# Kernel optimization log

Hardware: AMD Instinct MI355X
Metric: run time of the kernel (lower is better)

The kernel has to match this reference:

```python
import jax, jax.numpy as jnp
import numpy as np

N_NODES = 100000
N_EDGES = 1600000
IN_F, HID_F, OUT_F = 128, 128, 64


def setup_inputs() -> dict:
    key = jax.random.key(0)
    ks = jax.random.split(key, 8)
    x = jax.random.normal(ks[0], (N_NODES, IN_F), dtype=jnp.float32)
    edge_index = jax.random.randint(ks[1], (2, N_EDGES), 0, N_NODES, dtype=jnp.int64)
    w1 = jax.random.normal(ks[2], (IN_F, HID_F), dtype=jnp.float32) * 0.05
    b1 = jax.random.normal(ks[3], (HID_F,), dtype=jnp.float32) * 0.05
    c1 = jax.random.normal(ks[4], (IN_F, HID_F, 3), dtype=jnp.float32) * 0.01
    w2 = jax.random.normal(ks[5], (HID_F, OUT_F), dtype=jnp.float32) * 0.05
    b2 = jax.random.normal(ks[6], (OUT_F,), dtype=jnp.float32) * 0.05
    c2 = jax.random.normal(ks[7], (IN_F, OUT_F, 3), dtype=jnp.float32) * 0.01
    return {"x": x, "edge_index": edge_index, "w1": w1, "b1": b1, "c1": c1,
            "w2": w2, "b2": b2, "c2": c2}


def _minimal_kan(x, w, b, c):
    # linear term: (N, out)
    lin = x @ w + b
    # polynomial basis (x, x^2, x^3): (N, in, 3)
    basis = jnp.stack([x, x * x, x * x * x], axis=-1)
    # fused contraction over (in, 3); same math as the (N,in,out,3) broadcast-sum
    kan_out = jnp.einsum('nib,iob->no', basis, c)
    return lin + 0.1 * kan_out


def _aggregate(h, source, target, num_nodes):
    # mean over incoming messages, degree clamped at 1
    deg = jax.ops.segment_sum(jnp.ones(source.shape[0], dtype=h.dtype), target,
                              num_segments=num_nodes)
    deg = jnp.maximum(deg, 1.0)
    out = jax.ops.segment_sum(h[source], target, num_segments=num_nodes)
    return out / deg[:, None]


def reference(x, edge_index, w1, b1, c1, w2, b2, c2):
    source, target = edge_index[0], edge_index[1]
    n = x.shape[0]
    h = _minimal_kan(x, w1, b1, c1)
    h = jax.nn.relu(h)
    h = _aggregate(h, source, target, n)
    h = _minimal_kan(h, w2, b2, c2)
    h = _aggregate(h, source, target, n)
    return jax.nn.log_softmax(h, axis=-1)
```

## Files before the change

### kernel.cpp

```cpp
#include <hip/hip_runtime.h>
#include <hip/hip_bf16.h>
#include <math.h>

#define N_NODES 100000
#define N_EDGES 1600000
#define IN_F 128
#define HID_F 128
#define OUT_F 64
#define BSTX 136

#define BK_BITS 8
#define BK_SIZE 256
#define NBUCK ((N_NODES + BK_SIZE - 1) / BK_SIZE)
#define EPB 4096
#define NBLK_SORT ((N_EDGES + EPB - 1) / EPB)
#define BCAP 5120
#define PCAP (BCAP + 7 * BK_SIZE)
#define PK_SRC_MASK 0xffffffu
#define PAD8(d) (((d) + 7) & ~7)

#define K1T ((N_NODES + 63) / 64)
#define K1A 781
#define K1B (K1T - K1A)

#define K1_LDS (64 * BSTX * 2)
#define A_LDS 19520

typedef __attribute__((ext_vector_type(8))) short s8v;
typedef __attribute__((ext_vector_type(4))) short s4v;
typedef __attribute__((ext_vector_type(4))) float f4v;
typedef __attribute__((ext_vector_type(2))) float f2v;

__device__ __forceinline__ short f2bf(float f) {
    __hip_bfloat16 h = __float2bfloat16(f);
    return __builtin_bit_cast(short, h);
}
__device__ __forceinline__ float bf2f(short s) {
    return __builtin_bit_cast(float, ((unsigned)(unsigned short)s) << 16);
}

__global__ __launch_bounds__(256) void fold_weights_bf16(
    const float* __restrict__ w1, const float* __restrict__ c1,
    const float* __restrict__ w2, const float* __restrict__ c2,
    short* __restrict__ Wb1, short* __restrict__ Wb2,
    unsigned* __restrict__ h1d, unsigned* __restrict__ h2d,
    int* __restrict__ bcur)
{
    if (blockIdx.x == 0) {
        if (threadIdx.x < 32) h1d[(size_t)N_NODES * 32 + threadIdx.x] = 0;
        if (threadIdx.x < 16) h2d[(size_t)N_NODES * 16 + threadIdx.x] = 0;
        for (int i = threadIdx.x; i < NBUCK; i += 256) bcur[i] = i * BCAP;
    }
    int idx = blockIdx.x * 256 + threadIdx.x;
    if (idx < 384 * HID_F) {
        int k = idx >> 7, n = idx & 127;
        int p = k >> 7, f = k & 127;
        int si = f * HID_F + n;
        float v = (p == 0) ? (w1[si] + 0.1f * c1[si * 3])
                           : 0.1f * c1[si * 3 + p];
        Wb1[(((k >> 3) * HID_F) + n) * 8 + (k & 7)] = f2bf(v);
    } else {
        idx -= 384 * HID_F;
        if (idx < 384 * OUT_F) {
            int k = idx >> 6, n = idx & 63;
            int p = k >> 7, f = k & 127;
            int si = f * OUT_F + n;
            float v = (p == 0) ? (w2[si] + 0.1f * c2[si * 3])
                               : 0.1f * c2[si * 3 + p];
            Wb2[(((k >> 3) * OUT_F) + n) * 8 + (k & 7)] = f2bf(v);
        }
    }
}

__device__ __forceinline__ void kan1_body(
    short* sb, int node0,
    const float* __restrict__ x, const short* __restrict__ Wb,
    const float* __restrict__ bias, unsigned* __restrict__ h1d)
{
    const int tid  = threadIdx.x;
    const int lane = tid & 63;
    const int wave = tid >> 6;
    const int q = lane >> 4, r = lane & 15;

#pragma unroll
    for (int it = 0; it < 8; ++it) {
        int idx = tid + 256 * it;
        int m = idx >> 5, c4 = (idx & 31) * 4;
        int gm = min(node0 + m, N_NODES - 1);
        float4 v = *(const float4*)(x + (size_t)gm * IN_F + c4);
        s4v p0;
        p0[0] = f2bf(v.x); p0[1] = f2bf(v.y);
        p0[2] = f2bf(v.z); p0[3] = f2bf(v.w);
        *(s4v*)(sb + m * BSTX + c4) = p0;
    }
    __syncthreads();

    const int wm = (wave & 1) * 32;
    const int wn = (wave >> 1) * 64;

    f4v acc[2][4];
#pragma unroll
    for (int i = 0; i < 2; ++i)
#pragma unroll
        for (int j = 0; j < 4; ++j)
            acc[i][j] = (f4v){0.f, 0.f, 0.f, 0.f};

    float bj[4];
#pragma unroll
    for (int j = 0; j < 4; ++j) bj[j] = bias[wn + j * 16 + r];

#pragma unroll
    for (int kc = 0; kc < 4; ++kc) {
        const int col = kc * 32 + q * 8;
        s8v a0[2];
        float xf[2][8], x2[2][8];
#pragma unroll
        for (int i = 0; i < 2; ++i) {
            a0[i] = *(const s8v*)(sb + (wm + i * 16 + r) * BSTX + col);
#pragma unroll
            for (int t = 0; t < 8; ++t) xf[i][t] = bf2f(a0[i][t]);
        }
#pragma unroll
        for (int j = 0; j < 4; ++j) {
            const s8v b = *(const s8v*)(Wb + (((kc * 4 + q) * HID_F) + wn + j * 16 + r) * 8);
            acc[0][j] = __builtin_amdgcn_mfma_f32_16x16x32_bf16(a0[0], b, acc[0][j], 0, 0, 0);
            acc[1][j] = __builtin_amdgcn_mfma_f32_16x16x32_bf16(a0[1], b, acc[1][j], 0, 0, 0);
        }
        s8v a1[2];
#pragma unroll
        for (int i = 0; i < 2; ++i)
#pragma unroll
            for (int t = 0; t < 8; ++t) {
                x2[i][t] = xf[i][t] * xf[i][t];
                a1[i][t] = f2bf(x2[i][t]);
            }
#pragma unroll
        for (int j = 0; j < 4; ++j) {
            const s8v b = *(const s8v*)(Wb + ((((4 + kc) * 4 + q) * HID_F) + wn + j * 16 + r) * 8);
            acc[0][j] = __builtin_amdgcn_mfma_f32_16x16x32_bf16(a1[0], b, acc[0][j], 0, 0, 0);
            acc[1][j] = __builtin_amdgcn_mfma_f32_16x16x32_bf16(a1[1], b, acc[1][j], 0, 0, 0);
        }
        s8v a2[2];
#pragma unroll
        for (int i = 0; i < 2; ++i)
#pragma unroll
            for (int t = 0; t < 8; ++t)
                a2[i][t] = f2bf(x2[i][t] * xf[i][t]);
#pragma unroll
        for (int j = 0; j < 4; ++j) {
            const s8v b = *(const s8v*)(Wb + ((((8 + kc) * 4 + q) * HID_F) + wn + j * 16 + r) * 8);
            acc[0][j] = __builtin_amdgcn_mfma_f32_16x16x32_bf16(a2[0], b, acc[0][j], 0, 0, 0);
            acc[1][j] = __builtin_amdgcn_mfma_f32_16x16x32_bf16(a2[1], b, acc[1][j], 0, 0, 0);
        }
    }

    const int dci = ((wn >> 6) << 4) + r;
#pragma unroll
    for (int i = 0; i < 2; ++i)
#pragma unroll
        for (int e = 0; e < 4; ++e) {
            int grow = node0 + wm + i * 16 + q * 4 + e;
            if (grow < N_NODES) {
                float v0 = fmaxf(acc[i][0][e] + bj[0], 0.f);
                float v1 = fmaxf(acc[i][1][e] + bj[1], 0.f);
                float v2 = fmaxf(acc[i][2][e] + bj[2], 0.f);
                float v3 = fmaxf(acc[i][3][e] + bj[3], 0.f);
                int pk = __builtin_amdgcn_cvt_pk_fp8_f32(v0, v1, 0, false);
                pk = __builtin_amdgcn_cvt_pk_fp8_f32(v2, v3, pk, true);
                h1d[(size_t)grow * 32 + dci] = (unsigned)pk;
            }
        }
}

__global__ __launch_bounds__(256) void scatter_kan1(
    const int* __restrict__ src, const int* __restrict__ tgt,
    int* __restrict__ bcur, unsigned* __restrict__ spk,
    const float* __restrict__ x, const short* __restrict__ Wb,
    const float* __restrict__ bias, unsigned* __restrict__ h1d)
{
    __shared__ __align__(16) char smem[A_LDS];
    const int tid = threadIdx.x;

    if (blockIdx.x < NBLK_SORT) {
        int* h    = (int*)smem;
        int* base = h + NBUCK;
        int* tg   = base + NBUCK;
        for (int i = tid; i < NBUCK; i += 256) h[i] = 0;
        __syncthreads();
        int e0 = blockIdx.x * EPB;
        int n = min(EPB, N_EDGES - e0);
        for (int i = tid; i < n; i += 256) {
            int t = tgt[e0 + i];
            tg[i] = t;
            atomicAdd(&h[t >> BK_BITS], 1);
        }
        __syncthreads();
        for (int i = tid; i < NBUCK; i += 256) {
            int c = h[i];
            base[i] = c ? atomicAdd(&bcur[i], c) : 0;
            h[i] = 0;
        }
        __syncthreads();
        for (int i = tid; i < n; i += 256) {
            int t = tg[i];
            int b = t >> BK_BITS;
            int pos = base[b] + atomicAdd(&h[b], 1);
            spk[pos] = ((unsigned)(t - (b << BK_BITS)) << 24) | (unsigned)src[e0 + i];
        }
        return;
    }

    kan1_body((short*)smem, ((int)blockIdx.x - NBLK_SORT) * 64, x, Wb, bias, h1d);
}

__global__ __launch_bounds__(256) void csr_kan1(
    const int* __restrict__ bcur, const unsigned* __restrict__ spk,
    int* __restrict__ deg, int* __restrict__ prow, int* __restrict__ csr_pad,
    const float* __restrict__ x, const short* __restrict__ Wb,
    const float* __restrict__ bias, unsigned* __restrict__ h1d)
{
    __shared__ __align__(16) char smem[K1_LDS];
    const int tid = threadIdx.x;

    if (blockIdx.x < NBUCK) {
        int* d   = (int*)smem;
        int* pst = d + BK_SIZE;
        int* s   = pst + BK_SIZE;
        int b = blockIdx.x;
        d[tid] = 0;
        __syncthreads();
        int e0 = b * BCAP, e1 = bcur[b];
        for (int i = e0 + tid; i < e1; i += 256)
            atomicAdd(&d[spk[i] >> 24], 1);
        __syncthreads();
        int nbase = b << BK_BITS;
        int node = nbase + tid;
        int a = d[tid];
        if (node < N_NODES) deg[node] = a;
        int pc = (node < N_NODES) ? PAD8(a) : 0;
        s[tid] = pc;
        __syncthreads();
        for (int o = 1; o < 256; o <<= 1) {
            int t = (tid >= o) ? s[tid - o] : 0;
            __syncthreads();
            s[tid] += t;
            __syncthreads();
        }
        int excl = s[tid] - pc;
        int base = b * PCAP + excl;
        if (node < N_NODES) prow[node] = base;
        __syncthreads();
        d[tid] = base;
        pst[tid] = base + pc;
        __syncthreads();
        for (int i = e0 + tid; i < e1; i += 256) {
            unsigned pk = spk[i];
            int pos = atomicAdd(&d[pk >> 24], 1);
            csr_pad[pos] = (int)(pk & PK_SRC_MASK);
        }
        __syncthreads();
        {
            int kend = pst[tid];
            for (int k = d[tid]; k < kend; ++k) csr_pad[k] = N_NODES;
        }
        return;
    }

    kan1_body((short*)smem, (K1A + (int)blockIdx.x - NBUCK) * 64, x, Wb, bias, h1d);
}

__global__ __launch_bounds__(256) void gather128(
    const unsigned* __restrict__ h1d, const int* __restrict__ prow,
    const int* __restrict__ deg, const int* __restrict__ csr_pad,
    unsigned* __restrict__ a1d)
{
    const int lane  = threadIdx.x & 63;
    const int wave  = threadIdx.x >> 6;
    const int hl    = lane & 31;
    const int half  = lane >> 5;
    const int hbase = half << 5;
    const int node  = blockIdx.x * 8 + wave * 2 + half;

    int p0 = prow[node];
    int cnt = PAD8(deg[node]);
    int p1 = p0 + cnt;
    int cmax = max(cnt, __shfl_xor(cnt, 32));

    float acc[4][4];
#pragma unroll
    for (int t = 0; t < 4; ++t)
#pragma unroll
        for (int b = 0; b < 4; ++b) acc[t][b] = 0.f;

    for (int base = 0; base < cmax; base += 32) {
        int idx = max(min(p0 + base + hl, p1 - 1), 0);
        int sreg = csr_pad[idx];
        int lim = min(32, cmax - base);
        for (int j = 0; j < lim; j += 4) {
            if (base + j < cnt) {
                unsigned u[4];
#pragma unroll
                for (int t = 0; t < 4; ++t) {
                    int sj = __shfl(sreg, hbase + j + t);
                    u[t] = h1d[(size_t)sj * 32 + hl];
                }
#pragma unroll
                for (int t = 0; t < 4; ++t) {
                    f2v lo = __builtin_amdgcn_cvt_pk_f32_fp8(u[t], false);
                    f2v hi = __builtin_amdgcn_cvt_pk_f32_fp8(u[t], true);
                    acc[t][0] += lo.x; acc[t][1] += lo.y;
                    acc[t][2] += hi.x; acc[t][3] += hi.y;
                }
            }
        }
    }

    float s0 = (acc[0][0] + acc[1][0]) + (acc[2][0] + acc[3][0]);
    float s1 = (acc[0][1] + acc[1][1]) + (acc[2][1] + acc[3][1]);
    float s2 = (acc[0][2] + acc[1][2]) + (acc[2][2] + acc[3][2]);
    float s3 = (acc[0][3] + acc[1][3]) + (acc[2][3] + acc[3][3]);
    int pk = __builtin_amdgcn_cvt_pk_fp8_f32(s0, s1, 0, false);
    pk = __builtin_amdgcn_cvt_pk_fp8_f32(s2, s3, pk, true);
    a1d[(size_t)node * 32 + hl] = (unsigned)pk;
}

__global__ __launch_bounds__(256) void kan2_mfma(
    const unsigned* __restrict__ a1d, const int* __restrict__ deg,
    const short* __restrict__ Wb, const float* __restrict__ bias,
    unsigned short* __restrict__ h2s)
{
    __shared__ short sb[64 * BSTX];
    const int tid  = threadIdx.x;
    const int lane = tid & 63;
    const int wave = tid >> 6;
    const int node0 = blockIdx.x * 64;
    const int q = lane >> 4, r = lane & 15;

#pragma unroll
    for (int gi = 0; gi < 2; ++gi) {
        int g = tid + 256 * gi;
        int m = g >> 3, cg = (g & 7) * 4;
        int gm = min(node0 + m, N_NODES - 1);
        float di = 1.0f / fmaxf((float)deg[gm], 1.0f);
        uint4 u4 = *(const uint4*)(a1d + (size_t)gm * 32 + cg);
        unsigned uw[4] = {u4.x, u4.y, u4.z, u4.w};
        float xv[4][4];
#pragma unroll
        for (int j = 0; j < 4; ++j) {
            f2v lo = __builtin_amdgcn_cvt_pk_f32_fp8(uw[j], false);
            f2v hi = __builtin_amdgcn_cvt_pk_f32_fp8(uw[j], true);
            xv[j][0] = lo.x * di; xv[j][1] = lo.y * di;
            xv[j][2] = hi.x * di; xv[j][3] = hi.y * di;
        }
        int fb = ((cg >> 4) << 6) + (cg & 15);
#pragma unroll
        for (int b = 0; b < 4; ++b) {
            s4v p0;
#pragma unroll
            for (int j = 0; j < 4; ++j) p0[j] = f2bf(xv[j][b]);
            *(s4v*)(sb + m * BSTX + fb + 16 * b) = p0;
        }
    }
    __syncthreads();

    const int wm = (wave & 1) * 32;
    const int wn = (wave >> 1) * 32;

    f4v acc[2][2];
#pragma unroll
    for (int i = 0; i < 2; ++i)
#pragma unroll
        for (int j = 0; j < 2; ++j)
            acc[i][j] = (f4v){0.f, 0.f, 0.f, 0.f};

    float bj[2];
#pragma unroll
    for (int j = 0; j < 2; ++j) bj[j] = bias[wn + j * 16 + r];

#pragma unroll
    for (int kc = 0; kc < 4; ++kc) {
        const int col = kc * 32 + q * 8;
        s8v a0[2];
        float xf[2][8], x2[2][8];
#pragma unroll
        for (int i = 0; i < 2; ++i) {
            a0[i] = *(const s8v*)(sb + (wm + i * 16 + r) * BSTX + col);
#pragma unroll
            for (int t = 0; t < 8; ++t) xf[i][t] = bf2f(a0[i][t]);
        }
#pragma unroll
        for (int j = 0; j < 2; ++j) {
            const s8v b = *(const s8v*)(Wb + (((kc * 4 + q) * OUT_F) + wn + j * 16 + r) * 8);
            acc[0][j] = __builtin_amdgcn_mfma_f32_16x16x32_bf16(a0[0], b, acc[0][j], 0, 0, 0);
            acc[1][j] = __builtin_amdgcn_mfma_f32_16x16x32_bf16(a0[1], b, acc[1][j], 0, 0, 0);
        }
        s8v a1[2];
#pragma unroll
        for (int i = 0; i < 2; ++i)
#pragma unroll
            for (int t = 0; t < 8; ++t) {
                x2[i][t] = xf[i][t] * xf[i][t];
                a1[i][t] = f2bf(x2[i][t]);
            }
#pragma unroll
        for (int j = 0; j < 2; ++j) {
            const s8v b = *(const s8v*)(Wb + ((((4 + kc) * 4 + q) * OUT_F) + wn + j * 16 + r) * 8);
            acc[0][j] = __builtin_amdgcn_mfma_f32_16x16x32_bf16(a1[0], b, acc[0][j], 0, 0, 0);
            acc[1][j] = __builtin_amdgcn_mfma_f32_16x16x32_bf16(a1[1], b, acc[1][j], 0, 0, 0);
        }
        s8v a2[2];
#pragma unroll
        for (int i = 0; i < 2; ++i)
#pragma unroll
            for (int t = 0; t < 8; ++t)
                a2[i][t] = f2bf(x2[i][t] * xf[i][t]);
#pragma unroll
        for (int j = 0; j < 2; ++j) {
            const s8v b = *(const s8v*)(Wb + ((((8 + kc) * 4 + q) * OUT_F) + wn + j * 16 + r) * 8);
            acc[0][j] = __builtin_amdgcn_mfma_f32_16x16x32_bf16(a2[0], b, acc[0][j], 0, 0, 0);
            acc[1][j] = __builtin_amdgcn_mfma_f32_16x16x32_bf16(a2[1], b, acc[1][j], 0, 0, 0);
        }
    }

    const int sslot = (wn >> 1) + r;
#pragma unroll
    for (int i = 0; i < 2; ++i)
#pragma unroll
        for (int e = 0; e < 4; ++e) {
            int grow = node0 + wm + i * 16 + q * 4 + e;
            if (grow < N_NODES) {
                float vlo = acc[i][0][e] + bj[0];
                float vhi = acc[i][1][e] + bj[1];
                int pk = __builtin_amdgcn_cvt_pk_fp8_f32(vlo, vhi, 0, false);
                h2s[(size_t)grow * 32 + sslot] = (unsigned short)(pk & 0xffff);
            }
        }
}

__global__ __launch_bounds__(256) void gather64_lsm(
    const unsigned short* __restrict__ h2s, const int* __restrict__ deg,
    const int* __restrict__ prow, const int* __restrict__ csr_pad,
    float* __restrict__ out)
{
    const int lane = threadIdx.x & 63;
    const int wave = threadIdx.x >> 6;
    const int hl   = lane & 31;
    const int half = lane >> 5;
    const int node = blockIdx.x * 8 + wave * 2 + half;

    int p0 = prow[node];
    int degr = deg[node];
    int cnt = PAD8(degr);
    int p1 = p0 + cnt;
    int cmax = max(cnt, __shfl_xor(cnt, 32));

    float alo[8], ahi[8];
#pragma unroll
    for (int t = 0; t < 8; ++t) { alo[t] = 0.f; ahi[t] = 0.f; }

    for (int base = 0; base < cmax; base += 32) {
        int idx = max(min(p0 + base + hl, p1 - 1), 0);
        int sreg = csr_pad[idx];
        int lim = min(32, cmax - base);
        for (int j = 0; j < lim; j += 8) {
            if (base + j < cnt) {
                int u[8];
#pragma unroll
                for (int t = 0; t < 8; ++t) {
                    int sj = __shfl(sreg, (half << 5) + j + t);
                    u[t] = (int)h2s[(size_t)sj * 32 + hl];
                }
#pragma unroll
                for (int t = 0; t < 8; ++t) {
                    alo[t] += __builtin_amdgcn_cvt_f32_fp8(u[t], 0);
                    ahi[t] += __builtin_amdgcn_cvt_f32_fp8(u[t], 1);
                }
            }
        }
    }
    float slo = ((alo[0] + alo[1]) + (alo[2] + alo[3])) + ((alo[4] + alo[5]) + (alo[6] + alo[7]));
    float shi = ((ahi[0] + ahi[1]) + (ahi[2] + ahi[3])) + ((ahi[4] + ahi[5]) + (ahi[6] + ahi[7]));

    float di = 1.0f / fmaxf((float)degr, 1.0f);
    float vlo = slo * di, vhi = shi * di;

    float m = fmaxf(vlo, vhi);
#pragma unroll
    for (int off = 16; off >= 1; off >>= 1)
        m = fmaxf(m, __shfl_xor(m, off));
    float e = expf(vlo - m) + expf(vhi - m);
#pragma unroll
    for (int off = 16; off >= 1; off >>= 1)
        e += __shfl_xor(e, off);
    float ls = logf(e);

    const int f_lo = ((hl >> 4) << 5) + (hl & 15);
    out[(size_t)node * OUT_F + f_lo]      = vlo - m - ls;
    out[(size_t)node * OUT_F + f_lo + 16] = vhi - m - ls;
}

extern "C" void kernel_launch(void* const* d_in, const int* in_sizes, int n_in,
                              void* d_out, int out_size, void* d_ws, size_t ws_size,
                              hipStream_t stream)
{
    const float* x  = (const float*)d_in[0];
    const int*   ei = (const int*)d_in[1];
    const float* w1 = (const float*)d_in[2];
    const float* b1 = (const float*)d_in[3];
    const float* c1 = (const float*)d_in[4];
    const float* w2 = (const float*)d_in[5];
    const float* b2 = (const float*)d_in[6];
    const float* c2 = (const float*)d_in[7];
    float* out = (float*)d_out;

    const int* src = ei;
    const int* tgt = ei + N_EDGES;

    char* ws = (char*)d_ws;
    size_t off = 0;
    auto carve = [&](size_t bytes) -> void* {
        void* p = ws + off;
        off = (off + bytes + 255) & ~(size_t)255;
        return p;
    };
    short*    Wb1       = (short*)carve((size_t)384 * HID_F * 2);
    short*    Wb2       = (short*)carve((size_t)384 * OUT_F * 2);
    int*      deg       = (int*)carve((size_t)N_NODES * 4);
    int*      prow      = (int*)carve((size_t)N_NODES * 4);
    int*      bcur      = (int*)carve((size_t)NBUCK * 4);
    unsigned* spk       = (unsigned*)carve((size_t)NBUCK * BCAP * 4);
    int*      csr_pad   = (int*)carve((size_t)NBUCK * PCAP * 4);
    unsigned* h1d       = (unsigned*)carve(((size_t)N_NODES + 1) * 128);
    unsigned* a1d       = (unsigned*)carve((size_t)N_NODES * 128);
    unsigned short* h2s = (unsigned short*)carve(((size_t)N_NODES + 1) * 64);

    fold_weights_bf16<<<(384 * HID_F + 384 * OUT_F + 255) / 256, 256, 0, stream>>>(
        w1, c1, w2, c2, Wb1, Wb2, h1d, (unsigned*)h2s, bcur);

    scatter_kan1<<<NBLK_SORT + K1A, 256, 0, stream>>>(
        src, tgt, bcur, spk, x, Wb1, b1, h1d);

    csr_kan1<<<NBUCK + K1B, 256, 0, stream>>>(
        bcur, spk, deg, prow, csr_pad, x, Wb1, b1, h1d);

    gather128<<<(N_NODES + 7) / 8, 256, 0, stream>>>(h1d, prow, deg, csr_pad, a1d);

    kan2_mfma<<<(N_NODES + 63) / 64, 256, 0, stream>>>(a1d, deg, Wb2, b2, h2s);

    gather64_lsm<<<(N_NODES + 7) / 8, 256, 0, stream>>>(
        h2s, deg, prow, csr_pad, out);
}
```

Measured before the change: 231.7 us.

## Replace bucketed two-pass CSR build with global-atomic degree count, scan, and fill

New measurement: 334.6 us. 44.4% more time.

```diff
diff --git a/kernel.cpp b/kernel.cpp
--- a/kernel.cpp
+++ b/kernel.cpp
@@ -12,19 +12,18 @@
 #define BK_BITS 8
 #define BK_SIZE 256
 #define NBUCK ((N_NODES + BK_SIZE - 1) / BK_SIZE)
-#define EPB 4096
-#define NBLK_SORT ((N_EDGES + EPB - 1) / EPB)
-#define BCAP 5120
-#define PCAP (BCAP + 7 * BK_SIZE)
-#define PK_SRC_MASK 0xffffffu
+#define PCAP 6912
 #define PAD8(d) (((d) + 7) & ~7)
 
 #define K1T ((N_NODES + 63) / 64)
 #define K1A 781
 #define K1B (K1T - K1A)
 
+#define FOLD_BLKS 288
+#define CNT_BLKS 256
+#define FILL_BLKS 256
+
 #define K1_LDS (64 * BSTX * 2)
-#define A_LDS 19520
 
 typedef __attribute__((ext_vector_type(8))) short s8v;
 typedef __attribute__((ext_vector_type(4))) short s4v;
@@ -39,17 +38,28 @@
     return __builtin_bit_cast(float, ((unsigned)(unsigned short)s) << 16);
 }
 
-__global__ __launch_bounds__(256) void fold_weights_bf16(
+__global__ __launch_bounds__(256) void fold_count(
     const float* __restrict__ w1, const float* __restrict__ c1,
     const float* __restrict__ w2, const float* __restrict__ c2,
     short* __restrict__ Wb1, short* __restrict__ Wb2,
     unsigned* __restrict__ h1d, unsigned* __restrict__ h2d,
-    int* __restrict__ bcur)
-{
+    const int* __restrict__ tgt, int* __restrict__ deg)
+{
+    if (blockIdx.x >= FOLD_BLKS) {
+        int i0 = (blockIdx.x - FOLD_BLKS) * 256 + threadIdx.x;
+        const int4* t4 = (const int4*)tgt;
+        for (int i = i0; i < N_EDGES / 4; i += CNT_BLKS * 256) {
+            int4 t = t4[i];
+            atomicAdd(&deg[t.x], 1);
+            atomicAdd(&deg[t.y], 1);
+            atomicAdd(&deg[t.z], 1);
+            atomicAdd(&deg[t.w], 1);
+        }
+        return;
+    }
     if (blockIdx.x == 0) {
         if (threadIdx.x < 32) h1d[(size_t)N_NODES * 32 + threadIdx.x] = 0;
         if (threadIdx.x < 16) h2d[(size_t)N_NODES * 16 + threadIdx.x] = 0;
-        for (int i = threadIdx.x; i < NBUCK; i += 256) bcur[i] = i * BCAP;
     }
     int idx = blockIdx.x * 256 + threadIdx.x;
     if (idx < 384 * HID_F) {
@@ -172,72 +182,21 @@
         }
 }
 
-__global__ __launch_bounds__(256) void scatter_kan1(
-    const int* __restrict__ src, const int* __restrict__ tgt,
-    int* __restrict__ bcur, unsigned* __restrict__ spk,
+__global__ __launch_bounds__(256) void scan_kan1(
+    const int* __restrict__ deg, int* __restrict__ prow, int* __restrict__ cur,
+    int* __restrict__ csr_pad,
     const float* __restrict__ x, const short* __restrict__ Wb,
     const float* __restrict__ bias, unsigned* __restrict__ h1d)
 {
-    __shared__ __align__(16) char smem[A_LDS];
-    const int tid = threadIdx.x;
-
-    if (blockIdx.x < NBLK_SORT) {
-        int* h    = (int*)smem;
-        int* base = h + NBUCK;
-        int* tg   = base + NBUCK;
-        for (int i = tid; i < NBUCK; i += 256) h[i] = 0;
-        __syncthreads();
-        int e0 = blockIdx.x * EPB;
-        int n = min(EPB, N_EDGES - e0);
-        for (int i = tid; i < n; i += 256) {
-            int t = tgt[e0 + i];
-            tg[i] = t;
-            atomicAdd(&h[t >> BK_BITS], 1);
-        }
-        __syncthreads();
-        for (int i = tid; i < NBUCK; i += 256) {
-            int c = h[i];
-            base[i] = c ? atomicAdd(&bcur[i], c) : 0;
-            h[i] = 0;
-        }
-        __syncthreads();
-        for (int i = tid; i < n; i += 256) {
-            int t = tg[i];
-            int b = t >> BK_BITS;
-            int pos = base[b] + atomicAdd(&h[b], 1);
-            spk[pos] = ((unsigned)(t - (b << BK_BITS)) << 24) | (unsigned)src[e0 + i];
-        }
-        return;
-    }
-
-    kan1_body((short*)smem, ((int)blockIdx.x - NBLK_SORT) * 64, x, Wb, bias, h1d);
-}
-
-__global__ __launch_bounds__(256) void csr_kan1(
-    const int* __restrict__ bcur, const unsigned* __restrict__ spk,
-    int* __restrict__ deg, int* __restrict__ prow, int* __restrict__ csr_pad,
-    const float* __restrict__ x, const short* __restrict__ Wb,
-    const float* __restrict__ bias, unsigned* __restrict__ h1d)
-{
     __shared__ __align__(16) char smem[K1_LDS];
     const int tid = threadIdx.x;
 
     if (blockIdx.x < NBUCK) {
-        int* d   = (int*)smem;
-        int* pst = d + BK_SIZE;
-        int* s   = pst + BK_SIZE;
+        int* s = (int*)smem;
         int b = blockIdx.x;
-        d[tid] = 0;
-        __syncthreads();
-        int e0 = b * BCAP, e1 = bcur[b];
-        for (int i = e0 + tid; i < e1; i += 256)
-            atomicAdd(&d[spk[i] >> 24], 1);
-        __syncthreads();
-        int nbase = b << BK_BITS;
-        int node = nbase + tid;
-        int a = d[tid];
-        if (node < N_NODES) deg[node] = a;
-        int pc = (node < N_NODES) ? PAD8(a) : 0;
+        int node = (b << BK_BITS) + tid;
+        int d = (node < N_NODES) ? deg[node] : 0;
+        int pc = (node < N_NODES) ? PAD8(d) : 0;
         s[tid] = pc;
         __syncthreads();
         for (int o = 1; o < 256; o <<= 1) {
@@ -246,27 +205,41 @@
             s[tid] += t;
             __syncthreads();
         }
-        int excl = s[tid] - pc;
-        int base = b * PCAP + excl;
-        if (node < N_NODES) prow[node] = base;
-        __syncthreads();
-        d[tid] = base;
-        pst[tid] = base + pc;
-        __syncthreads();
-        for (int i = e0 + tid; i < e1; i += 256) {
-            unsigned pk = spk[i];
-            int pos = atomicAdd(&d[pk >> 24], 1);
-            csr_pad[pos] = (int)(pk & PK_SRC_MASK);
-        }
-        __syncthreads();
-        {
-            int kend = pst[tid];
-            for (int k = d[tid]; k < kend; ++k) csr_pad[k] = N_NODES;
+        int base = b * PCAP + s[tid] - pc;
+        if (node < N_NODES) {
+            prow[node] = base;
+            cur[node]  = base;
+            for (int k = base + d; k < base + pc; ++k) csr_pad[k] = N_NODES;
         }
         return;
     }
 
-    kan1_body((short*)smem, (K1A + (int)blockIdx.x - NBUCK) * 64, x, Wb, bias, h1d);
+    kan1_body((short*)smem, ((int)blockIdx.x - NBUCK) * 64, x, Wb, bias, h1d);
+}
+
+__global__ __launch_bounds__(256) void fill_kan1(
+    const int* __restrict__ src, const int* __restrict__ tgt,
+    int* __restrict__ cur, int* __restrict__ csr_pad,
+    const float* __restrict__ x, const short* __restrict__ Wb,
+    const float* __restrict__ bias, unsigned* __restrict__ h1d)
+{
+    __shared__ __align__(16) char smem[K1_LDS];
+    if (blockIdx.x < FILL_BLKS) {
+        int i0 = blockIdx.x * 256 + threadIdx.x;
+        const int4* t4 = (const int4*)tgt;
+        const int4* s4 = (const int4*)src;
+        for (int i = i0; i < N_EDGES / 4; i += FILL_BLKS * 256) {
+            int4 t = t4[i];
+            int4 s = s4[i];
+            csr_pad[atomicAdd(&cur[t.x], 1)] = s.x;
+            csr_pad[atomicAdd(&cur[t.y], 1)] = s.y;
+            csr_pad[atomicAdd(&cur[t.z], 1)] = s.z;
+            csr_pad[atomicAdd(&cur[t.w], 1)] = s.w;
+        }
+        return;
+    }
+
+    kan1_body((short*)smem, (K1A + (int)blockIdx.x - FILL_BLKS) * 64, x, Wb, bias, h1d);
 }
 
 __global__ __launch_bounds__(256) void gather128(
@@ -527,21 +500,22 @@
     short*    Wb2       = (short*)carve((size_t)384 * OUT_F * 2);
     int*      deg       = (int*)carve((size_t)N_NODES * 4);
     int*      prow      = (int*)carve((size_t)N_NODES * 4);
-    int*      bcur      = (int*)carve((size_t)NBUCK * 4);
-    unsigned* spk       = (unsigned*)carve((size_t)NBUCK * BCAP * 4);
+    int*      cur       = (int*)carve((size_t)N_NODES * 4);
     int*      csr_pad   = (int*)carve((size_t)NBUCK * PCAP * 4);
     unsigned* h1d       = (unsigned*)carve(((size_t)N_NODES + 1) * 128);
     unsigned* a1d       = (unsigned*)carve((size_t)N_NODES * 128);
     unsigned short* h2s = (unsigned short*)carve(((size_t)N_NODES + 1) * 64);
 
-    fold_weights_bf16<<<(384 * HID_F + 384 * OUT_F + 255) / 256, 256, 0, stream>>>(
-        w1, c1, w2, c2, Wb1, Wb2, h1d, (unsigned*)h2s, bcur);
-
-    scatter_kan1<<<NBLK_SORT + K1A, 256, 0, stream>>>(
-        src, tgt, bcur, spk, x, Wb1, b1, h1d);
-
-    csr_kan1<<<NBUCK + K1B, 256, 0, stream>>>(
-        bcur, spk, deg, prow, csr_pad, x, Wb1, b1, h1d);
+    hipMemsetAsync(deg, 0, (size_t)N_NODES * 4, stream);
+
+    fold_count<<<FOLD_BLKS + CNT_BLKS, 256, 0, stream>>>(
+        w1, c1, w2, c2, Wb1, Wb2, h1d, (unsigned*)h2s, tgt, deg);
+
+    scan_kan1<<<NBUCK + K1A, 256, 0, stream>>>(
+        deg, prow, cur, csr_pad, x, Wb1, b1, h1d);
+
+    fill_kan1<<<FILL_BLKS + K1B, 256, 0, stream>>>(
+        src, tgt, cur, csr_pad, x, Wb1, b1, h1d);
 
     gather128<<<(N_NODES + 7) / 8, 256, 0, stream>>>(h1d, prow, deg, csr_pad, a1d);
 
```

## Interleave sort and KAN1 blocks, overlap second-half gather with first-half KAN2

Applied to the files above, without the earlier changes.

Measured after the change: 237.6 us. +2.5%, slower.

```diff
diff --git a/kernel.cpp b/kernel.cpp
--- a/kernel.cpp
+++ b/kernel.cpp
@@ -16,12 +16,18 @@
 #define NBLK_SORT ((N_EDGES + EPB - 1) / EPB)
 #define BCAP 5120
 #define PCAP (BCAP + 7 * BK_SIZE)
+#define PK_SHIFT 24
 #define PK_SRC_MASK 0xffffffu
 #define PAD8(d) (((d) + 7) & ~7)
 
 #define K1T ((N_NODES + 63) / 64)
 #define K1A 781
 #define K1B (K1T - K1A)
+
+#define G1A_BLKS 6256
+#define G1B_BLKS (12500 - G1A_BLKS)
+#define K2A_BLKS 782
+#define K2B_BLKS (K1T - K2A_BLKS)
 
 #define K1_LDS (64 * BSTX * 2)
 #define A_LDS 19520
@@ -180,14 +186,16 @@
 {
     __shared__ __align__(16) char smem[A_LDS];
     const int tid = threadIdx.x;
-
-    if (blockIdx.x < NBLK_SORT) {
+    const int sgrp = blockIdx.x / 3;
+    const int r3   = blockIdx.x % 3;
+
+    if (r3 == 0) {
         int* h    = (int*)smem;
         int* base = h + NBUCK;
         int* tg   = base + NBUCK;
         for (int i = tid; i < NBUCK; i += 256) h[i] = 0;
         __syncthreads();
-        int e0 = blockIdx.x * EPB;
+        int e0 = sgrp * EPB;
         int n = min(EPB, N_EDGES - e0);
         for (int i = tid; i < n; i += 256) {
             int t = tgt[e0 + i];
@@ -205,12 +213,12 @@
             int t = tg[i];
             int b = t >> BK_BITS;
             int pos = base[b] + atomicAdd(&h[b], 1);
-            spk[pos] = ((unsigned)(t - (b << BK_BITS)) << 24) | (unsigned)src[e0 + i];
+            spk[pos] = ((unsigned)(t - (b << BK_BITS)) << PK_SHIFT) | (unsigned)src[e0 + i];
         }
         return;
     }
 
-    kan1_body((short*)smem, ((int)blockIdx.x - NBLK_SORT) * 64, x, Wb, bias, h1d);
+    kan1_body((short*)smem, (2 * sgrp + r3 - 1) * 64, x, Wb, bias, h1d);
 }
 
 __global__ __launch_bounds__(256) void csr_kan1(
@@ -221,20 +229,21 @@
 {
     __shared__ __align__(16) char smem[K1_LDS];
     const int tid = threadIdx.x;
-
-    if (blockIdx.x < NBUCK) {
+    const int sgrp = blockIdx.x / 3;
+    const int r3   = blockIdx.x % 3;
+
+    if (r3 == 0) {
         int* d   = (int*)smem;
         int* pst = d + BK_SIZE;
         int* s   = pst + BK_SIZE;
-        int b = blockIdx.x;
+        int b = sgrp;
         d[tid] = 0;
         __syncthreads();
         int e0 = b * BCAP, e1 = bcur[b];
         for (int i = e0 + tid; i < e1; i += 256)
-            atomicAdd(&d[spk[i] >> 24], 1);
-        __syncthreads();
-        int nbase = b << BK_BITS;
-        int node = nbase + tid;
+            atomicAdd(&d[spk[i] >> PK_SHIFT], 1);
+        __syncthreads();
+        int node = (b << BK_BITS) + tid;
         int a = d[tid];
         if (node < N_NODES) deg[node] = a;
         int pc = (node < N_NODES) ? PAD8(a) : 0;
@@ -255,7 +264,7 @@
         __syncthreads();
         for (int i = e0 + tid; i < e1; i += 256) {
             unsigned pk = spk[i];
-            int pos = atomicAdd(&d[pk >> 24], 1);
+            int pos = atomicAdd(&d[pk >> PK_SHIFT], 1);
             csr_pad[pos] = (int)(pk & PK_SRC_MASK);
         }
         __syncthreads();
@@ -266,11 +275,11 @@
         return;
     }
 
-    kan1_body((short*)smem, (K1A + (int)blockIdx.x - NBUCK) * 64, x, Wb, bias, h1d);
-}
-
-__global__ __launch_bounds__(256) void gather128(
-    const unsigned* __restrict__ h1d, const int* __restrict__ prow,
+    kan1_body((short*)smem, (K1A + 2 * sgrp + r3 - 1) * 64, x, Wb, bias, h1d);
+}
+
+__device__ __forceinline__ void gather128_body(
+    int blk, const unsigned* __restrict__ h1d, const int* __restrict__ prow,
     const int* __restrict__ deg, const int* __restrict__ csr_pad,
     unsigned* __restrict__ a1d)
 {
@@ -279,7 +288,7 @@
     const int hl    = lane & 31;
     const int half  = lane >> 5;
     const int hbase = half << 5;
-    const int node  = blockIdx.x * 8 + wave * 2 + half;
+    const int node  = blk * 8 + wave * 2 + half;
 
     int p0 = prow[node];
     int cnt = PAD8(deg[node]);
@@ -324,16 +333,15 @@
     a1d[(size_t)node * 32 + hl] = (unsigned)pk;
 }
 
-__global__ __launch_bounds__(256) void kan2_mfma(
+__device__ __forceinline__ void kan2_body(
+    short* sb, int node0,
     const unsigned* __restrict__ a1d, const int* __restrict__ deg,
     const short* __restrict__ Wb, const float* __restrict__ bias,
     unsigned short* __restrict__ h2s)
 {
-    __shared__ short sb[64 * BSTX];
     const int tid  = threadIdx.x;
     const int lane = tid & 63;
     const int wave = tid >> 6;
-    const int node0 = blockIdx.x * 64;
     const int q = lane >> 4, r = lane & 15;
 
 #pragma unroll
@@ -435,6 +443,38 @@
                 h2s[(size_t)grow * 32 + sslot] = (unsigned short)(pk & 0xffff);
             }
         }
+}
+
+__global__ __launch_bounds__(256) void gather128_a(
+    const unsigned* __restrict__ h1d, const int* __restrict__ prow,
+    const int* __restrict__ deg, const int* __restrict__ csr_pad,
+    unsigned* __restrict__ a1d)
+{
+    gather128_body(blockIdx.x, h1d, prow, deg, csr_pad, a1d);
+}
+
+__global__ __launch_bounds__(256, 8) void g1b_kan2a(
+    const unsigned* __restrict__ h1d, const int* __restrict__ prow,
+    const int* __restrict__ deg, const int* __restrict__ csr_pad,
+    unsigned* __restrict__ a1d,
+    const short* __restrict__ Wb, const float* __restrict__ bias,
+    unsigned short* __restrict__ h2s)
+{
+    __shared__ short sb[64 * BSTX];
+    if (blockIdx.x < K2A_BLKS) {
+        kan2_body(sb, blockIdx.x * 64, a1d, deg, Wb, bias, h2s);
+        return;
+    }
+    gather128_body(G1A_BLKS + (int)blockIdx.x - K2A_BLKS, h1d, prow, deg, csr_pad, a1d);
+}
+
+__global__ __launch_bounds__(256) void kan2_b(
+    const unsigned* __restrict__ a1d, const int* __restrict__ deg,
+    const short* __restrict__ Wb, const float* __restrict__ bias,
+    unsigned short* __restrict__ h2s)
+{
+    __shared__ short sb[64 * BSTX];
+    kan2_body(sb, (K2A_BLKS + (int)blockIdx.x) * 64, a1d, deg, Wb, bias, h2s);
 }
 
 __global__ __launch_bounds__(256) void gather64_lsm(
@@ -540,12 +580,15 @@
     scatter_kan1<<<NBLK_SORT + K1A, 256, 0, stream>>>(
         src, tgt, bcur, spk, x, Wb1, b1, h1d);
 
-    csr_kan1<<<NBUCK + K1B, 256, 0, stream>>>(
+    csr_kan1<<<3 * NBUCK, 256, 0, stream>>>(
         bcur, spk, deg, prow, csr_pad, x, Wb1, b1, h1d);
 
-    gather128<<<(N_NODES + 7) / 8, 256, 0, stream>>>(h1d, prow, deg, csr_pad, a1d);
-
-    kan2_mfma<<<(N_NODES + 63) / 64, 256, 0, stream>>>(a1d, deg, Wb2, b2, h2s);
+    gather128_a<<<G1A_BLKS, 256, 0, stream>>>(h1d, prow, deg, csr_pad, a1d);
+
+    g1b_kan2a<<<K2A_BLKS + G1B_BLKS, 256, 0, stream>>>(
+        h1d, prow, deg, csr_pad, a1d, Wb2, b2, h2s);
+
+    kan2_b<<<K2B_BLKS, 256, 0, stream>>>(a1d, deg, Wb2, b2, h2s);
 
     gather64_lsm<<<(N_NODES + 7) / 8, 256, 0, stream>>>(
         h2s, deg, prow, csr_pad, out);
```
